# Optimization experiments

Hardware: AMD Instinct MI355X
Metric: run time of the kernel (lower is better)

## Reference

```python
import jax, jax.numpy as jnp
import numpy as np


def _cdist(x, y):
    # Euclidean pairwise distances, (N,D) x (M,D) -> (N,M)
    x2 = jnp.sum(x * x, axis=1, keepdims=True)          # (N,1)
    y2 = jnp.sum(y * y, axis=1, keepdims=True).T        # (1,M)
    sq = x2 + y2 - 2.0 * (x @ y.T)
    return jnp.sqrt(jnp.maximum(sq, 0.0))


def setup_inputs() -> dict:
    key = jax.random.key(0)
    k1, k2, k3, k4 = jax.random.split(key, 4)
    return {
        "pred_feat": jax.random.normal(k1, (8192, 6), dtype=jnp.float32),
        "pred_decoder": jax.random.normal(k2, (4096, 4), dtype=jnp.float32),
        "input_data": jax.random.normal(k3, (4096, 4), dtype=jnp.float32),
        "gt_data": jax.random.normal(k4, (32768, 6), dtype=jnp.float32),
    }


def _repulsion_loss(pred_points, alpha=100.0, margin=0.3):
    N = pred_points.shape[0]
    d = _cdist(pred_points, pred_points)                # (N,N)
    eye = jnp.eye(N, dtype=d.dtype)
    d_no_self = d + 1e6 * eye
    min_dist = jnp.min(d_no_self, axis=1)               # (N,)
    penalty = jax.nn.softplus(alpha * (margin - min_dist))
    return jnp.mean(penalty ** 2)


def reference(pred_feat, pred_decoder, input_data, gt_data):
    # train_decoder=False branch of CombinedCriterionAEImpulse.forward
    pred_points = pred_feat[:, :3]
    pred_normals = pred_feat[:, 3:]
    gt_points = gt_data[:, :3]
    gt_normals = gt_data[:, 3:]

    # nearest-neighbor matching: NxL cdist + argmin + gather
    dists = _cdist(pred_points, gt_points)              # (N,L)
    min_indices = jnp.argmin(dists, axis=1)             # (N,)
    closest_gt_points = gt_points[min_indices]          # (N,3)

    attraction_loss = jnp.mean((pred_points - closest_gt_points) ** 2)
    repulsion = _repulsion_loss(pred_points)
    inlier_loss = attraction_loss + repulsion

    # normal alignment loss
    closest_gt_normals = gt_normals[min_indices]        # (N,3)
    eps = 1e-05
    pn = pred_normals / jnp.maximum(
        jnp.linalg.norm(pred_normals, axis=1, keepdims=True), eps)
    gn = closest_gt_normals / jnp.maximum(
        jnp.linalg.norm(closest_gt_normals, axis=1, keepdims=True), eps)
    cos_theta = jnp.sum(pn * gn, axis=1)
    norm_loss = jnp.mean(1.0 - cos_theta)

    combined_loss = inlier_loss + norm_loss * 10.0
    return combined_loss
```

## Files before the change

### kernel.cpp

```cpp
#include <hip/hip_runtime.h>
#include <cstdint>

typedef unsigned short ushort_t;
typedef unsigned int u32;
typedef unsigned long long u64;
typedef __attribute__((ext_vector_type(8))) short bf16x8;
typedef __attribute__((ext_vector_type(16))) float f32x16;

#define N_PRED 8192
#define N_GT   32768

#define NN_WAVES  4096
#define ALL_WAVES 5120

#define O_PRA  1048576u
#define O_PRB  1310720u
#define O_KNN  1572864u
#define O_KRP  5767168u
#define O_PART 6815744u

__device__ __forceinline__ float max3f(float a, float b, float c) {
    float d;
    asm("v_max3_f32 %0, %1, %2, %3" : "=v"(d) : "v"(a), "v"(b), "v"(c));
    return d;
}
__device__ __forceinline__ ushort_t f2b(float v) {
    u32 b = __float_as_uint(v);
    return (ushort_t)((b + 0x7FFFu + ((b >> 16) & 1u)) >> 16);
}
__device__ __forceinline__ u32 packf(float v) {
    const u32 b = __float_as_uint(v);
    return b ^ ((u32)((int)b >> 31) | 0x80000000u);
}
__device__ __forceinline__ float red16(const f32x16 a, float best) {
    const float m0 = max3f(a[0], a[1], a[2]);
    const float m1 = max3f(a[3], a[4], a[5]);
    const float m2 = max3f(a[6], a[7], a[8]);
    const float m3 = max3f(a[9], a[10], a[11]);
    const float m4 = max3f(a[12], a[13], a[14]);
    const float m5 = max3f(m0, m1, a[15]);
    const float m6 = max3f(m2, m3, m4);
    return max3f(best, m5, m6);
}

#define MASKROW(ACC)                                               \
    {                                                              \
        _Pragma("unroll")                                          \
        for (int _r = 0; _r < 16; ++_r) {                          \
            const int _row = (_r & 3) + 8 * (_r >> 2) + rowoff;    \
            ACC[_r] = (_row == col) ? -3.0e38f : ACC[_r];          \
        }                                                          \
    }

__global__ __launch_bounds__(256) void k_prep(const float* __restrict__ pred,
                                              const float* __restrict__ gt,
                                              ushort_t* __restrict__ gtA,
                                              ushort_t* __restrict__ prA,
                                              ushort_t* __restrict__ prB) {
    const int i = blockIdx.x * 256 + threadIdx.x;
    if (i < N_GT) {
        const float x = gt[i * 6 + 0], y = gt[i * 6 + 1], z = gt[i * 6 + 2];
        const ushort_t xh = f2b(x), yh = f2b(y), zh = f2b(z);
        const ushort_t xl = f2b(x - __uint_as_float((u32)xh << 16));
        const ushort_t yl = f2b(y - __uint_as_float((u32)yh << 16));
        const ushort_t zl = f2b(z - __uint_as_float((u32)zh << 16));
        const float w = -0.5f * fmaf(z, z, fmaf(y, y, x * x));
        const ushort_t wh = f2b(w);
        const ushort_t wl = f2b(w - __uint_as_float((u32)wh << 16));
        ushort_t* d = gtA + (i >> 5) * 512 + (i & 31) * 8;
        d[0] = xh; d[1] = yh; d[2] = zh; d[3] = xh; d[4] = yh; d[5] = zh; d[6] = xl; d[7] = yl;
        d += 256;
        d[0] = zl; d[1] = wh; d[2] = wl; d[3] = 0; d[4] = 0; d[5] = 0; d[6] = 0; d[7] = 0;
    }
    if (i < N_PRED) {
        const float x = pred[i * 6 + 0], y = pred[i * 6 + 1], z = pred[i * 6 + 2];
        const ushort_t xh = f2b(x), yh = f2b(y), zh = f2b(z);
        const ushort_t xl = f2b(x - __uint_as_float((u32)xh << 16));
        const ushort_t yl = f2b(y - __uint_as_float((u32)yh << 16));
        const ushort_t zl = f2b(z - __uint_as_float((u32)zh << 16));
        const float w = -0.5f * fmaf(z, z, fmaf(y, y, x * x));
        const ushort_t wh = f2b(w);
        const ushort_t wl = f2b(w - __uint_as_float((u32)wh << 16));
        ushort_t* a = prA + (i >> 5) * 512 + (i & 31) * 8;
        a[0] = xh; a[1] = yh; a[2] = zh; a[3] = xh; a[4] = yh; a[5] = zh; a[6] = xl; a[7] = yl;
        a += 256;
        a[0] = zl; a[1] = wh; a[2] = wl; a[3] = 0; a[4] = 0; a[5] = 0; a[6] = 0; a[7] = 0;
        const ushort_t ONE = 0x3F80;
        ushort_t* b = prB + (i >> 5) * 512 + (i & 31) * 8;
        b[0] = xh; b[1] = yh; b[2] = zh; b[3] = xl; b[4] = yl; b[5] = zl; b[6] = xh; b[7] = yh;
        b += 256;
        b[0] = zh; b[1] = ONE; b[2] = ONE; b[3] = 0; b[4] = 0; b[5] = 0; b[6] = 0; b[7] = 0;
    }
}

template <bool DIAG>
__device__ __forceinline__ void scan16(const bf16x8* __restrict__ ap,
                                       const bf16x8 B0, const bf16x8 B1,
                                       const bf16x8 B2, const bf16x8 B3,
                                       const int ts0, const int ts1,
                                       const int ts2, const int ts3,
                                       const int col, const int rowoff,
                                       float& b0, float& b1, float& b2, float& b3,
                                       u32& k0, u32& k1, u32& k2, u32& k3) {
    const f32x16 zc = {};
    bf16x8 Acur = ap[0];
#pragma unroll
    for (int G = 0; G < 4; ++G) {
        float g0 = -3.0e38f, g1 = -3.0e38f, g2 = -3.0e38f, g3 = -3.0e38f;
#pragma unroll
        for (int tt = 0; tt < 4; ++tt) {
            const int t = G * 4 + tt;
            const bf16x8 Anxt = (t < 15) ? ap[(t + 1) * 64] : Acur;
            f32x16 accA = __builtin_amdgcn_mfma_f32_32x32x16_bf16(Acur, B0, zc, 0, 0, 0);
            f32x16 accB = __builtin_amdgcn_mfma_f32_32x32x16_bf16(Acur, B1, zc, 0, 0, 0);
            if (DIAG && t == ts0) MASKROW(accA);
            g0 = red16(accA, g0);
            accA = __builtin_amdgcn_mfma_f32_32x32x16_bf16(Acur, B2, zc, 0, 0, 0);
            if (DIAG && t == ts1) MASKROW(accB);
            g1 = red16(accB, g1);
            accB = __builtin_amdgcn_mfma_f32_32x32x16_bf16(Acur, B3, zc, 0, 0, 0);
            if (DIAG && t == ts2) MASKROW(accA);
            g2 = red16(accA, g2);
            if (DIAG && t == ts3) MASKROW(accB);
            g3 = red16(accB, g3);
            Acur = Anxt;
        }
        k0 = (g0 > b0) ? (u32)G : k0;  b0 = fmaxf(b0, g0);
        k1 = (g1 > b1) ? (u32)G : k1;  b1 = fmaxf(b1, g1);
        k2 = (g2 > b2) ? (u32)G : k2;  b2 = fmaxf(b2, g2);
        k3 = (g3 > b3) ? (u32)G : k3;  b3 = fmaxf(b3, g3);
    }
}

__global__ __launch_bounds__(256) void k_pair(const ushort_t* __restrict__ gtA,
                                              const ushort_t* __restrict__ prA,
                                              const ushort_t* __restrict__ prB,
                                              u64* __restrict__ keysNN,
                                              u64* __restrict__ keysRP) {
    const int wid = blockIdx.x * 4 + (threadIdx.x >> 6);
    const int lane = threadIdx.x & 63;

    const bool isNN = (wid < NN_WAVES);
    const int rw = isNN ? wid : (wid - NN_WAVES);
    const int pg = rw & 63;
    const int sp = rw >> 6;

    const int col = lane & 31;
    const int rowoff = (lane >> 5) * 4;

    const bf16x8* bp = (const bf16x8*)prB;
    const bf16x8 B0 = bp[(pg * 4 + 0) * 64 + lane];
    const bf16x8 B1 = bp[(pg * 4 + 1) * 64 + lane];
    const bf16x8 B2 = bp[(pg * 4 + 2) * 64 + lane];
    const bf16x8 B3 = bp[(pg * 4 + 3) * 64 + lane];

    const bf16x8* ap = (const bf16x8*)(isNN ? gtA : prA) + sp * 1024 + lane;

    float b0 = -3.0e38f, b1 = -3.0e38f, b2 = -3.0e38f, b3 = -3.0e38f;
    u32 k0 = 0, k1 = 0, k2 = 0, k3 = 0;

    const bool diag = (!isNN) && (sp == (pg >> 2));
    if (diag) {
        const int tb = (pg & 3) * 4;
        scan16<true>(ap, B0, B1, B2, B3, tb, tb + 1, tb + 2, tb + 3,
                     col, rowoff, b0, b1, b2, b3, k0, k1, k2, k3);
    } else {
        scan16<false>(ap, B0, B1, B2, B3, -1, -1, -1, -1,
                      col, rowoff, b0, b1, b2, b3, k0, k1, k2, k3);
    }

#define FOLD(B, K)                                                  \
    {                                                               \
        const float _ob = __shfl_xor(B, 32);                        \
        const u32 _ok = __shfl_xor(K, 32);                          \
        const bool _tk = (_ob > B) || (_ob == B && _ok < K);        \
        B = _tk ? _ob : B;                                          \
        K = _tk ? _ok : K;                                          \
    }
    FOLD(b0, k0); FOLD(b1, k1); FOLD(b2, k2); FOLD(b3, k3);
#undef FOLD

    if (lane < 32) {
        u64* keys = isNN ? keysNN : keysRP;
        const int Pb = pg * 128 + col;
        const u32 gb = (u32)(sp * 4);
        keys[(size_t)sp * N_PRED + Pb +  0] = ((u64)packf(b0) << 32) | (u64)(~(gb + k0));
        keys[(size_t)sp * N_PRED + Pb + 32] = ((u64)packf(b1) << 32) | (u64)(~(gb + k1));
        keys[(size_t)sp * N_PRED + Pb + 64] = ((u64)packf(b2) << 32) | (u64)(~(gb + k2));
        keys[(size_t)sp * N_PRED + Pb + 96] = ((u64)packf(b3) << 32) | (u64)(~(gb + k3));
    }
}

__global__ __launch_bounds__(256) void k_fin(const float* __restrict__ pred,
                                             const float* __restrict__ gt,
                                             const u64* __restrict__ keysNN,
                                             const u64* __restrict__ keysRP,
                                             float* __restrict__ partials) {
    const int wave = threadIdx.x >> 6;
    const int lane = threadIdx.x & 63;
    const int p = blockIdx.x * 4 + wave;

    const float px = pred[p * 6 + 0], py = pred[p * 6 + 1], pz = pred[p * 6 + 2];

    u64 kv = keysNN[(size_t)lane * N_PRED + p];
#pragma unroll
    for (int off = 32; off > 0; off >>= 1) {
        const u64 o = __shfl_xor(kv, off);
        kv = (o > kv) ? o : kv;
    }
    const int G = (int)(~(u32)kv);
    float bh = -3.0e38f;
    int bj = 0x7FFFFFFF;
#pragma unroll
    for (int i = 0; i < 2; ++i) {
        const int g = G * 128 + i * 64 + lane;
        const float x = gt[g * 6 + 0], y = gt[g * 6 + 1], z = gt[g * 6 + 2];
        const float w = -0.5f * fmaf(z, z, fmaf(y, y, x * x));
        const float h = fmaf(px, x, fmaf(py, y, fmaf(pz, z, w)));
        if (h > bh) { bh = h; bj = g; }
    }
#pragma unroll
    for (int off = 32; off > 0; off >>= 1) {
        const float oh = __shfl_xor(bh, off);
        const int og = __shfl_xor(bj, off);
        const bool take = (oh > bh) || (oh == bh && og < bj);
        bh = take ? oh : bh;
        bj = take ? og : bj;
    }
    const int j = bj;

    u64 rv = (lane < 16) ? keysRP[(size_t)lane * N_PRED + p] : 0ull;
#pragma unroll
    for (int off = 32; off > 0; off >>= 1) {
        const u64 o = __shfl_xor(rv, off);
        rv = (o > rv) ? o : rv;
    }
    const int G2 = (int)(~(u32)rv);
    float hr = -3.0e38f;
#pragma unroll
    for (int i = 0; i < 2; ++i) {
        const int q = G2 * 128 + i * 64 + lane;
        const float x = pred[q * 6 + 0], y = pred[q * 6 + 1], z = pred[q * 6 + 2];
        const float w = -0.5f * fmaf(z, z, fmaf(y, y, x * x));
        float h = fmaf(px, x, fmaf(py, y, fmaf(pz, z, w)));
        h = (q == p) ? -3.0e38f : h;
        hr = fmaxf(hr, h);
    }
#pragma unroll
    for (int off = 32; off > 0; off >>= 1) hr = fmaxf(hr, __shfl_xor(hr, off));

    __shared__ float red[4][3];
    if (lane == 0) {
        const float gx = gt[j * 6 + 0], gy = gt[j * 6 + 1], gz = gt[j * 6 + 2];
        const float dx = px - gx, dy = py - gy, dz = pz - gz;
        const float att = dx * dx + dy * dy + dz * dz;

        const float pnx = pred[p * 6 + 3], pny = pred[p * 6 + 4], pnz = pred[p * 6 + 5];
        const float gnx = gt[j * 6 + 3],   gny = gt[j * 6 + 4],   gnz = gt[j * 6 + 5];
        const float pl = fmaxf(sqrtf(pnx * pnx + pny * pny + pnz * pnz), 1e-5f);
        const float gl = fmaxf(sqrtf(gnx * gnx + gny * gny + gnz * gnz), 1e-5f);
        const float nrm = 1.0f - (pnx * gnx + pny * gny + pnz * gnz) / (pl * gl);

        const float pp2 = px * px + py * py + pz * pz;
        float d2 = fmaf(-2.0f, hr, pp2);
        d2 = fmaxf(d2, 0.0f);
        const float xa = 100.0f * (0.3f - sqrtf(d2));
        const float sp2 = fmaxf(xa, 0.0f) + log1pf(expf(-fabsf(xa)));

        red[wave][0] = att;
        red[wave][1] = nrm;
        red[wave][2] = sp2 * sp2;
    }
    __syncthreads();
    if (threadIdx.x < 3)
        partials[blockIdx.x * 3 + threadIdx.x] =
            red[0][threadIdx.x] + red[1][threadIdx.x] +
            red[2][threadIdx.x] + red[3][threadIdx.x];
}

__device__ __forceinline__ float wave_reduce(float v) {
#pragma unroll
    for (int off = 32; off > 0; off >>= 1) v += __shfl_down(v, off, 64);
    return v;
}

__global__ __launch_bounds__(256) void k_comb(const float* __restrict__ partials,
                                              float* __restrict__ out) {
    float a = 0.f, n = 0.f, r = 0.f;
    const int t = threadIdx.x;
#pragma unroll
    for (int k = 0; k < 8; ++k) {
        const int row = t + k * 256;
        a += partials[row * 3 + 0];
        n += partials[row * 3 + 1];
        r += partials[row * 3 + 2];
    }
    a = wave_reduce(a);
    n = wave_reduce(n);
    r = wave_reduce(r);
    __shared__ float red[3][4];
    const int wave = t >> 6, lane = t & 63;
    if (lane == 0) { red[0][wave] = a; red[1][wave] = n; red[2][wave] = r; }
    __syncthreads();
    if (t == 0) {
        const float A = red[0][0] + red[0][1] + red[0][2] + red[0][3];
        const float Nn = red[1][0] + red[1][1] + red[1][2] + red[1][3];
        const float R = red[2][0] + red[2][1] + red[2][2] + red[2][3];
        out[0] = A / (float)(N_PRED * 3) + R / (float)N_PRED + 10.0f * (Nn / (float)N_PRED);
    }
}

extern "C" void kernel_launch(void* const* d_in, const int* in_sizes, int n_in,
                              void* d_out, int out_size, void* d_ws, size_t ws_size,
                              hipStream_t stream) {
    const float* pred = (const float*)d_in[0];
    const float* gt   = (const float*)d_in[3];
    float* out = (float*)d_out;
    char* ws = (char*)d_ws;

    ushort_t* gtA = (ushort_t*)ws;
    ushort_t* prA = (ushort_t*)(ws + O_PRA);
    ushort_t* prB = (ushort_t*)(ws + O_PRB);
    u64* keysNN = (u64*)(ws + O_KNN);
    u64* keysRP = (u64*)(ws + O_KRP);
    float* partials = (float*)(ws + O_PART);

    k_prep<<<N_GT / 256, 256, 0, stream>>>(pred, gt, gtA, prA, prB);
    k_pair<<<ALL_WAVES / 4, 256, 0, stream>>>(gtA, prA, prB, keysNN, keysRP);
    k_fin<<<N_PRED / 4, 256, 0, stream>>>(pred, gt, keysNN, keysRP, partials);
    k_comb<<<1, 256, 0, stream>>>(partials, out);
}
```

Measured before the change: 39.59 us.

## Fuse bf16 split-packing prep into pair kernel with LDS-staged A tiles

Removes the separate prep kernel and its workspace round-trip. Each block of the pair kernel now converts its 512-point slice of gt or pred into hi/lo bf16 fragments in shared memory, while each wave builds its B fragments for four pred groups directly in registers. The four waves in a block share one LDS A tile, not each loading A from global memory. This saves one launch and the global write/read of packed arrays, at the cost of redundant per-block conversion work and a block barrier before the MFMA scan.

```diff
diff --git a/kernel.cpp b/kernel.cpp
--- a/kernel.cpp
+++ b/kernel.cpp
@@ -10,14 +10,11 @@
 #define N_PRED 8192
 #define N_GT   32768
 
-#define NN_WAVES  4096
-#define ALL_WAVES 5120
-
-#define O_PRA  1048576u
-#define O_PRB  1310720u
-#define O_KNN  1572864u
-#define O_KRP  5767168u
-#define O_PART 6815744u
+#define NN_BLOCKS 1024
+#define RP_BLOCKS 256
+
+#define O_KRP  4194304u
+#define O_PART 5242880u
 
 __device__ __forceinline__ float max3f(float a, float b, float c) {
     float d;
@@ -27,6 +24,9 @@
 __device__ __forceinline__ ushort_t f2b(float v) {
     u32 b = __float_as_uint(v);
     return (ushort_t)((b + 0x7FFFu + ((b >> 16) & 1u)) >> 16);
+}
+__device__ __forceinline__ float b2f(ushort_t h) {
+    return __uint_as_float((u32)h << 16);
 }
 __device__ __forceinline__ u32 packf(float v) {
     const u32 b = __float_as_uint(v);
@@ -51,47 +51,6 @@
             ACC[_r] = (_row == col) ? -3.0e38f : ACC[_r];          \
         }                                                          \
     }
-
-__global__ __launch_bounds__(256) void k_prep(const float* __restrict__ pred,
-                                              const float* __restrict__ gt,
-                                              ushort_t* __restrict__ gtA,
-                                              ushort_t* __restrict__ prA,
-                                              ushort_t* __restrict__ prB) {
-    const int i = blockIdx.x * 256 + threadIdx.x;
-    if (i < N_GT) {
-        const float x = gt[i * 6 + 0], y = gt[i * 6 + 1], z = gt[i * 6 + 2];
-        const ushort_t xh = f2b(x), yh = f2b(y), zh = f2b(z);
-        const ushort_t xl = f2b(x - __uint_as_float((u32)xh << 16));
-        const ushort_t yl = f2b(y - __uint_as_float((u32)yh << 16));
-        const ushort_t zl = f2b(z - __uint_as_float((u32)zh << 16));
-        const float w = -0.5f * fmaf(z, z, fmaf(y, y, x * x));
-        const ushort_t wh = f2b(w);
-        const ushort_t wl = f2b(w - __uint_as_float((u32)wh << 16));
-        ushort_t* d = gtA + (i >> 5) * 512 + (i & 31) * 8;
-        d[0] = xh; d[1] = yh; d[2] = zh; d[3] = xh; d[4] = yh; d[5] = zh; d[6] = xl; d[7] = yl;
-        d += 256;
-        d[0] = zl; d[1] = wh; d[2] = wl; d[3] = 0; d[4] = 0; d[5] = 0; d[6] = 0; d[7] = 0;
-    }
-    if (i < N_PRED) {
-        const float x = pred[i * 6 + 0], y = pred[i * 6 + 1], z = pred[i * 6 + 2];
-        const ushort_t xh = f2b(x), yh = f2b(y), zh = f2b(z);
-        const ushort_t xl = f2b(x - __uint_as_float((u32)xh << 16));
-        const ushort_t yl = f2b(y - __uint_as_float((u32)yh << 16));
-        const ushort_t zl = f2b(z - __uint_as_float((u32)zh << 16));
-        const float w = -0.5f * fmaf(z, z, fmaf(y, y, x * x));
-        const ushort_t wh = f2b(w);
-        const ushort_t wl = f2b(w - __uint_as_float((u32)wh << 16));
-        ushort_t* a = prA + (i >> 5) * 512 + (i & 31) * 8;
-        a[0] = xh; a[1] = yh; a[2] = zh; a[3] = xh; a[4] = yh; a[5] = zh; a[6] = xl; a[7] = yl;
-        a += 256;
-        a[0] = zl; a[1] = wh; a[2] = wl; a[3] = 0; a[4] = 0; a[5] = 0; a[6] = 0; a[7] = 0;
-        const ushort_t ONE = 0x3F80;
-        ushort_t* b = prB + (i >> 5) * 512 + (i & 31) * 8;
-        b[0] = xh; b[1] = yh; b[2] = zh; b[3] = xl; b[4] = yl; b[5] = zl; b[6] = xh; b[7] = yh;
-        b += 256;
-        b[0] = zh; b[1] = ONE; b[2] = ONE; b[3] = 0; b[4] = 0; b[5] = 0; b[6] = 0; b[7] = 0;
-    }
-}
 
 template <bool DIAG>
 __device__ __forceinline__ void scan16(const bf16x8* __restrict__ ap,
@@ -132,50 +91,87 @@
     }
 }
 
-__global__ __launch_bounds__(256) void k_pair(const ushort_t* __restrict__ gtA,
-                                              const ushort_t* __restrict__ prA,
-                                              const ushort_t* __restrict__ prB,
+__global__ __launch_bounds__(256) void k_pair(const float* __restrict__ pred,
+                                              const float* __restrict__ gt,
                                               u64* __restrict__ keysNN,
                                               u64* __restrict__ keysRP) {
-    const int wid = blockIdx.x * 4 + (threadIdx.x >> 6);
+    __shared__ bf16x8 As[1024];
+    const int w = threadIdx.x >> 6;
     const int lane = threadIdx.x & 63;
-
-    const bool isNN = (wid < NN_WAVES);
-    const int rw = isNN ? wid : (wid - NN_WAVES);
-    const int pg = rw & 63;
-    const int sp = rw >> 6;
+    const int b = blockIdx.x;
+    const bool isNN = (b < NN_BLOCKS);
+    const int pgBase = isNN ? (b >> 6) : ((b - NN_BLOCKS) >> 4);
+    const int sp     = isNN ? (b & 63) : ((b - NN_BLOCKS) & 15);
+    const int pg = pgBase * 4 + w;
+
+    const float* __restrict__ src = isNN ? gt : pred;
+#pragma unroll
+    for (int k = 0; k < 2; ++k) {
+        const int idx = k * 256 + threadIdx.x;
+        const int gidx = sp * 512 + idx;
+        const float x = src[gidx * 6 + 0], y = src[gidx * 6 + 1], z = src[gidx * 6 + 2];
+        const ushort_t xh = f2b(x), yh = f2b(y), zh = f2b(z);
+        const ushort_t xl = f2b(x - b2f(xh));
+        const ushort_t yl = f2b(y - b2f(yh));
+        const ushort_t zl = f2b(z - b2f(zh));
+        const float wv = -0.5f * fmaf(z, z, fmaf(y, y, x * x));
+        const ushort_t wh = f2b(wv);
+        const ushort_t wl = f2b(wv - b2f(wh));
+        bf16x8 h0, h1;
+        h0[0] = (short)xh; h0[1] = (short)yh; h0[2] = (short)zh; h0[3] = (short)xh;
+        h0[4] = (short)yh; h0[5] = (short)zh; h0[6] = (short)xl; h0[7] = (short)yl;
+        h1[0] = (short)zl; h1[1] = (short)wh; h1[2] = (short)wl; h1[3] = 0;
+        h1[4] = 0; h1[5] = 0; h1[6] = 0; h1[7] = 0;
+        const int t = idx >> 5, row_ = idx & 31;
+        As[t * 64 + row_] = h0;
+        As[t * 64 + 32 + row_] = h1;
+    }
 
     const int col = lane & 31;
-    const int rowoff = (lane >> 5) * 4;
-
-    const bf16x8* bp = (const bf16x8*)prB;
-    const bf16x8 B0 = bp[(pg * 4 + 0) * 64 + lane];
-    const bf16x8 B1 = bp[(pg * 4 + 1) * 64 + lane];
-    const bf16x8 B2 = bp[(pg * 4 + 2) * 64 + lane];
-    const bf16x8 B3 = bp[(pg * 4 + 3) * 64 + lane];
-
-    const bf16x8* ap = (const bf16x8*)(isNN ? gtA : prA) + sp * 1024 + lane;
-
+    const int kh = lane >> 5;
+    const int rowoff = kh * 4;
+    const ushort_t ONE = 0x3F80;
+    bf16x8 B[4];
+#pragma unroll
+    for (int j = 0; j < 4; ++j) {
+        const int p = pg * 128 + j * 32 + col;
+        const float x = pred[p * 6 + 0], y = pred[p * 6 + 1], z = pred[p * 6 + 2];
+        const ushort_t xh = f2b(x), yh = f2b(y), zh = f2b(z);
+        const ushort_t xl = f2b(x - b2f(xh));
+        const ushort_t yl = f2b(y - b2f(yh));
+        const ushort_t zl = f2b(z - b2f(zh));
+        B[j][0] = (short)(kh ? zh : xh);
+        B[j][1] = (short)(kh ? ONE : yh);
+        B[j][2] = (short)(kh ? ONE : zh);
+        B[j][3] = (short)(kh ? 0 : xl);
+        B[j][4] = (short)(kh ? 0 : yl);
+        B[j][5] = (short)(kh ? 0 : zl);
+        B[j][6] = (short)(kh ? 0 : xh);
+        B[j][7] = (short)(kh ? 0 : yh);
+    }
+    __syncthreads();
+
+    const bf16x8* ap = &As[lane];
     float b0 = -3.0e38f, b1 = -3.0e38f, b2 = -3.0e38f, b3 = -3.0e38f;
     u32 k0 = 0, k1 = 0, k2 = 0, k3 = 0;
 
-    const bool diag = (!isNN) && (sp == (pg >> 2));
+    const bool diag = (!isNN) && (sp == pgBase);
     if (diag) {
-        const int tb = (pg & 3) * 4;
-        scan16<true>(ap, B0, B1, B2, B3, tb, tb + 1, tb + 2, tb + 3,
+        const int tb = w * 4;
+        scan16<true>(ap, B[0], B[1], B[2], B[3], tb, tb + 1, tb + 2, tb + 3,
                      col, rowoff, b0, b1, b2, b3, k0, k1, k2, k3);
     } else {
-        scan16<false>(ap, B0, B1, B2, B3, -1, -1, -1, -1,
+        scan16<false>(ap, B[0], B[1], B[2], B[3], -1, -1, -1, -1,
                       col, rowoff, b0, b1, b2, b3, k0, k1, k2, k3);
     }
 
-#define FOLD(B, K)                                                  \
+#define FOLD(B_, K_)                                                \
     {                                                               \
-        const float _ob = __shfl_xor(B, 32);                        \
-        const u32 _ok = __shfl_xor(K, 32);                          \
-        const bool _tk = (_ob > B) || (_ob == B && _ok < K);        \
-        B = _tk ? _ob : B;                                          \
-        K = _tk ? _ok : K;                                          \
+        const float _ob = __shfl_xor(B_, 32);                       \
+        const u32 _ok = __shfl_xor(K_, 32);                         \
+        const bool _tk = (_ob > B_) || (_ob == B_ && _ok < K_);     \
+        B_ = _tk ? _ob : B_;                                        \
+        K_ = _tk ? _ok : K_;                                        \
     }
     FOLD(b0, k0); FOLD(b1, k1); FOLD(b2, k2); FOLD(b3, k3);
 #undef FOLD
@@ -318,15 +314,11 @@
     float* out = (float*)d_out;
     char* ws = (char*)d_ws;
 
-    ushort_t* gtA = (ushort_t*)ws;
-    ushort_t* prA = (ushort_t*)(ws + O_PRA);
-    ushort_t* prB = (ushort_t*)(ws + O_PRB);
-    u64* keysNN = (u64*)(ws + O_KNN);
+    u64* keysNN = (u64*)ws;
     u64* keysRP = (u64*)(ws + O_KRP);
     float* partials = (float*)(ws + O_PART);
 
-    k_prep<<<N_GT / 256, 256, 0, stream>>>(pred, gt, gtA, prA, prB);
-    k_pair<<<ALL_WAVES / 4, 256, 0, stream>>>(gtA, prA, prB, keysNN, keysRP);
+    k_pair<<<NN_BLOCKS + RP_BLOCKS, 256, 0, stream>>>(pred, gt, keysNN, keysRP);
     k_fin<<<N_PRED / 4, 256, 0, stream>>>(pred, gt, keysNN, keysRP, partials);
     k_comb<<<1, 256, 0, stream>>>(partials, out);
 }
```

New measurement: 35.54 us, median of 2. 10.2% less time.
